# Performance work log

Measured on AMD Instinct MI355X. Metric: run time of the kernel, lower is better.

The kernel has to match this reference:

```python
import jax, jax.numpy as jnp
import numpy as np
from math import comb

N, D, ORDER, P = 32768, 8, 19, 20
O = ORDER + 1


def bernstein(X, order):
    # X: [N, D] in [0,1] -> Bernstein basis [N, D, order+1]
    o = order + 1
    r = jnp.arange(o, dtype=X.dtype)
    binom = jnp.asarray([comb(order, k) for k in range(o)], dtype=X.dtype)
    Xe = X[..., None]
    return (Xe ** r) * ((1.0 - Xe) ** (order - r)) * binom


def setup_inputs() -> dict:
    key = jax.random.key(0)
    k0, k1, k2, k3, k4, k5 = jax.random.split(key, 6)
    X = jax.random.uniform(k0, (N, D), dtype=jnp.float32)
    # perm: each row is a permutation of range(D) (as in the module default)
    perm = jax.vmap(lambda k: jax.random.permutation(k, D))(jax.random.split(k1, P)).astype(jnp.int32)
    meanw0 = -0.2 + 0.1 * jax.random.normal(k2, (P, 1, O), dtype=jnp.float32)
    meanw = -0.2 + 0.1 * jax.random.normal(k3, (D - 1, P, O, O), dtype=jnp.float32)
    varw0 = 0.05 * jax.random.normal(k4, (P, 1, O), dtype=jnp.float32)
    varw = 0.05 * jax.random.normal(k5, (D - 1, P, O, O), dtype=jnp.float32)
    return {"X": X, "perm": perm, "meanw0": meanw0, "meanw": meanw,
            "varw0": varw0, "varw": varw}


def reference(X, perm, meanw0, meanw, varw0, varw):
    outB = bernstein(X, ORDER)                       # [N, D, O]
    outBp = jnp.transpose(outB[:, perm], (1, 0, 2, 3))  # gather axis=1 -> [P, N, D, O]

    # ---- f_mean: chain of small matmuls with exp(meanw_i), gated by basis ----
    f = jnp.exp(meanw0) * outBp[:, :, 0, :]          # [P,1,O]*[P,N,O] -> [P,N,O]
    for i in range(1, D):
        f = jnp.einsum('pno,poq->pnq', f, jnp.exp(meanw[i - 1])) * outBp[:, :, i, :]
    mean = jnp.sum(jnp.sum(f, axis=-1), axis=0)[:, None]   # [N,1]

    # ---- f_var: six moment chains one..six, exp(meanw)^2 * exp(varw)^k ----
    kk = jnp.arange(1, 7, dtype=X.dtype).reshape(6, 1, 1, 1)
    B2_0 = outBp[:, :, 0, :] ** 2                    # [P,N,O]
    acc = jnp.exp(2.0 * meanw0 + kk * varw0) * B2_0[None]  # [6,P,N,O]
    for i in range(1, D):
        Wi = jnp.exp(2.0 * meanw[i - 1] + kk * varw[i - 1])  # [6,P,O,O]
        acc = jnp.einsum('kpno,kpoq->kpnq', acc, Wi) * (outBp[:, :, i, :] ** 2)[None]
    mom = jnp.sum(acc, axis=-1)                      # [6,P,N]
    c = jnp.asarray([1.0, 1 / 2, 1 / 6, 1 / 24, 1 / 120, 1 / 720], dtype=X.dtype)
    var = jnp.einsum('k,kpn->n', c, mom)[:, None]    # [N,1]

    return jnp.concatenate([mean, var], axis=-1)     # [N,2]
```

## Files before the change

### kernel.cpp

```cpp
#include <hip/hip_runtime.h>
#include <math.h>

#define NPTS 32768
#define DD 8
#define OO 20
#define PP 20
#define NCHAIN 7
#define NT 2

typedef _Float16 half8 __attribute__((ext_vector_type(8)));
typedef __fp16 fp16x2 __attribute__((ext_vector_type(2)));
typedef float floatx16 __attribute__((ext_vector_type(16)));
typedef unsigned int u32;

#define AS1 __attribute__((address_space(1)))
#define AS3 __attribute__((address_space(3)))

__device__ __forceinline__ int sigma_row(int m) {
    return (m >= 4 && m < 12) ? (m ^ 12) : m;
}

__device__ __forceinline__ void basis20(float tv, float* g) {
    constexpr float binom[OO] = {
        1.f, 19.f, 171.f, 969.f, 3876.f, 11628.f, 27132.f, 50388.f, 75582.f,
        92378.f, 92378.f, 75582.f, 50388.f, 27132.f, 11628.f, 3876.f, 969.f,
        171.f, 19.f, 1.f};
    float a = tv, b = 1.f - tv, v = 1.f;
#pragma unroll
    for (int q = 0; q < OO; ++q) { g[q] = v; v *= a; }
    v = 1.f;
#pragma unroll
    for (int q = OO - 1; q >= 0; --q) { g[q] = g[q] * v * binom[q]; v *= b; }
}

__device__ __forceinline__ unsigned pk2rtn(float a, float b) {
    union { _Float16 h[2]; unsigned u; } cv;
    cv.h[0] = (_Float16)a; cv.h[1] = (_Float16)b;
    return cv.u;
}

__device__ __forceinline__ unsigned pack_pk(float x, float y) {
    union { fp16x2 h; unsigned u; } cv;
    cv.h = __builtin_amdgcn_cvt_pkrtz(x, y);
    return cv.u;
}

__device__ __forceinline__ fp16x2 u2h(unsigned u) {
    union { unsigned u; fp16x2 h; } c; c.u = u; return c.h;
}
__device__ __forceinline__ unsigned h2u(fp16x2 h) {
    union { unsigned u; fp16x2 h; } c; c.h = h; return c.u;
}

__global__ void zero_kernel(float4* __restrict__ out) {
    int e = blockIdx.x * 256 + threadIdx.x;
    out[e] = make_float4(0.f, 0.f, 0.f, 0.f);
}

__global__ void prep_kernel(const float* __restrict__ X,
                            const float* __restrict__ meanw0,
                            const float* __restrict__ meanw,
                            const float* __restrict__ varw0,
                            const float* __restrict__ varw,
                            float* __restrict__ W0,
                            _Float16* __restrict__ WA,
                            unsigned* __restrict__ G) {
    int e = blockIdx.x * 256 + threadIdx.x;
    const int n0 = NCHAIN * PP * OO;
    const int nW = NCHAIN * (DD - 1) * PP * 32 * 32;
    const int nG = NPTS * DD;
    if (e < n0) {
        int q = e % OO;
        int rem = e / OO;
        int p = rem % PP;
        int c = rem / PP;
        float m = meanw0[p * OO + q];
        W0[e] = (c == 0) ? __expf(m) : __expf(2.f * m + (float)c * varw0[p * OO + q]);
    } else if (e < n0 + nW) {
        int idx = e - n0;
        int j = idx & 7; idx >>= 3;
        int l = idx & 63; idx >>= 6;
        int f = idx & 1; idx >>= 1;
        int p = idx % PP; idx /= PP;
        int i = idx % (DD - 1);
        int c = idx / (DD - 1);
        int m = l & 31;
        int k = (l >> 5) * 8 + f * 16 + j;
        int q = sigma_row(m);
        float v = 0.f;
        if (q < OO && k < OO) {
            int mi = ((i * PP + p) * OO + k) * OO + q;
            float mm = meanw[mi];
            v = (c == 0) ? __expf(mm) : __expf(2.f * mm + (float)c * varw[mi]);
        }
        WA[e - n0] = (_Float16)v;
    } else if (e < n0 + nW + nG) {
        int idx = e - n0 - nW;
        int n = idx & (NPTS - 1);
        int d = idx >> 15;
        float g[OO];
        basis20(X[(size_t)n * DD + d], g);
        uint4 o0, o1, o2;
        o0.x = pk2rtn(g[0], g[1]);
        o0.y = pk2rtn(g[2], g[3]);
        o0.z = pk2rtn(g[4], g[5]);
        o0.w = pk2rtn(g[6], g[7]);
        o1.x = pk2rtn(g[16], g[17]);
        o1.y = pk2rtn(g[18], g[19]);
        o1.z = pk2rtn(g[8], g[9]);
        o1.w = pk2rtn(g[10], g[11]);
        o2.x = pk2rtn(g[12], g[13]);
        o2.y = pk2rtn(g[14], g[15]);
        o2.z = 0u;
        o2.w = 0u;
        uint4* out = (uint4*)(G + (size_t)(d * NPTS + n) * 12);
        out[0] = o0; out[1] = o1; out[2] = o2;
    }
}

__global__ __launch_bounds__(256, 2) void chain_kernel(
    const int* __restrict__ perm,
    const float* __restrict__ W0, const _Float16* __restrict__ WA,
    const unsigned* __restrict__ G, float* __restrict__ out) {
    const int lane = threadIdx.x & 63;
    const int wv = threadIdx.x >> 6;
    const int nl = lane & 31;
    const bool hi = (lane >> 5) != 0;
    const int n0 = (blockIdx.x * 4 + wv) * (32 * NT);
    const int p = blockIdx.y;
    const int goffd = hi ? 6 : 0;

    __shared__ __align__(16) _Float16 Alds[2][NCHAIN * 1024];

    int dp[DD];
#pragma unroll
    for (int i = 0; i < DD; ++i) dp[i] = perm[p * DD + i];

    const unsigned uz = ((unsigned)dp[0]) >> 20;
    const float fz = __uint_as_float(uz);
    floatx16 kZero;
#pragma unroll
    for (int r = 0; r < 16; ++r) kZero[r] = fz;

    {
        const _Float16* wbase = WA + (size_t)p * 1024;
#pragma unroll
        for (int u = wv; u < 2 * NCHAIN; u += 4) {
            int c = u >> 1, h = u & 1;
            const _Float16* src =
                wbase + (size_t)c * (DD - 1) * PP * 1024 + h * 512 + lane * 8;
            __builtin_amdgcn_global_load_lds(
                (const AS1 u32*)src, (AS3 u32*)&Alds[0][u * 512], 16, 0, 0);
        }
    }

    unsigned st[NT][NCHAIN][6];

#pragma unroll
    for (int tile = 0; tile < NT; ++tile) {
        const uint2* rp = (const uint2*)(
            G + ((size_t)dp[0] * NPTS + (n0 + tile * 32 + nl)) * 12 + goffd);
        uint2 r0 = rp[0], r1 = rp[1], r2 = rp[2];
        unsigned gw[6] = {r0.x, r0.y, r1.x, r1.y, r2.x, r2.y};
        float gcf[12], scf[12];
#pragma unroll
        for (int q = 0; q < 6; ++q) {
            fp16x2 gh = u2h(gw[q]);
            gcf[2 * q] = (float)gh.x; gcf[2 * q + 1] = (float)gh.y;
        }
#pragma unroll
        for (int r = 0; r < 12; ++r) scf[r] = gcf[r] * gcf[r];
#pragma unroll
        for (int c = 0; c < NCHAIN; ++c) {
            const float* w0r = W0 + (c * PP + p) * OO;
            float val[12];
#pragma unroll
            for (int r = 0; r < 8; ++r) {
                float ws = hi ? w0r[r + 8] : w0r[r];
                val[r] = ws * (c == 0 ? gcf[r] : scf[r]);
            }
#pragma unroll
            for (int r = 8; r < 12; ++r) {
                float ws = hi ? 0.f : w0r[r + 8];
                val[r] = ws * (c == 0 ? gcf[r] : scf[r]);
            }
#pragma unroll
            for (int e = 0; e < 6; ++e)
                st[tile][c][e] = pack_pk(val[2 * e], val[2 * e + 1]);
        }
    }

    const float coef[NCHAIN] = {0.f, 1.f, 0.5f, 1.f / 6.f, 1.f / 24.f,
                                1.f / 120.f, 1.f / 720.f};
    float sm[NT], sv[NT];
#pragma unroll
    for (int tile = 0; tile < NT; ++tile) { sm[tile] = 0.f; sv[tile] = 0.f; }

    __syncthreads();

#pragma unroll
    for (int i = 1; i < DD; ++i) {
        const int cur = (i - 1) & 1;

        if (i < DD - 1) {
            const _Float16* wbase = WA + (size_t)(i * PP + p) * 1024;
#pragma unroll
            for (int u = wv; u < 2 * NCHAIN; u += 4) {
                int c = u >> 1, h = u & 1;
                const _Float16* src =
                    wbase + (size_t)c * (DD - 1) * PP * 1024 + h * 512 + lane * 8;
                __builtin_amdgcn_global_load_lds(
                    (const AS1 u32*)src, (AS3 u32*)&Alds[cur ^ 1][u * 512], 16, 0, 0);
            }
        }

        unsigned gw[NT][6], sw[NT][6];
#pragma unroll
        for (int tile = 0; tile < NT; ++tile) {
            const uint2* rp = (const uint2*)(
                G + ((size_t)dp[i] * NPTS + (n0 + tile * 32 + nl)) * 12 + goffd);
            uint2 r0 = rp[0], r1 = rp[1], r2 = rp[2];
            gw[tile][0] = r0.x; gw[tile][1] = r0.y;
            gw[tile][2] = r1.x; gw[tile][3] = r1.y;
            gw[tile][4] = r2.x; gw[tile][5] = r2.y;
        }
        if (i < DD - 1) {
#pragma unroll
            for (int tile = 0; tile < NT; ++tile)
#pragma unroll
                for (int e = 0; e < 6; ++e) {
                    fp16x2 gh = u2h(gw[tile][e]);
                    sw[tile][e] = h2u(gh * gh);
                }
        }

        float gcf[NT][12], scf[NT][12];
        if (i == DD - 1) {
#pragma unroll
            for (int tile = 0; tile < NT; ++tile) {
#pragma unroll
                for (int q = 0; q < 6; ++q) {
                    fp16x2 gh = u2h(gw[tile][q]);
                    gcf[tile][2 * q] = (float)gh.x; gcf[tile][2 * q + 1] = (float)gh.y;
                }
#pragma unroll
                for (int r = 0; r < 12; ++r)
                    scf[tile][r] = gcf[tile][r] * gcf[tile][r];
            }
        }

#pragma unroll
        for (int c = 0; c < NCHAIN; ++c) {
            const _Float16* ab = &Alds[cur][c * 1024 + lane * 8];
            half8 A0 = *(const half8*)(ab);
            half8 A1 = *(const half8*)(ab + 512);

#pragma unroll
            for (int tile = 0; tile < NT; ++tile) {
                union { unsigned u[4]; half8 h; } B0, B1;
                B0.u[0] = st[tile][c][0]; B0.u[1] = st[tile][c][1];
                B0.u[2] = st[tile][c][2]; B0.u[3] = st[tile][c][3];
                B1.u[0] = st[tile][c][4]; B1.u[1] = st[tile][c][5];
                B1.u[2] = uz;             B1.u[3] = uz;

                floatx16 acc;
                acc = __builtin_amdgcn_mfma_f32_32x32x16_f16(A0, B0.h, kZero, 0, 0, 0);
                acc = __builtin_amdgcn_mfma_f32_32x32x16_f16(A1, B1.h, acc, 0, 0, 0);

                if (i < DD - 1) {
#pragma unroll
                    for (int e = 0; e < 6; ++e) {
                        fp16x2 pr = __builtin_amdgcn_cvt_pkrtz(acc[2 * e], acc[2 * e + 1]);
                        fp16x2 gv = u2h(c == 0 ? gw[tile][e] : sw[tile][e]);
                        st[tile][c][e] = h2u(pr * gv);
                    }
                } else {
                    float s = 0.f;
#pragma unroll
                    for (int r = 0; r < 12; ++r)
                        s += acc[r] * (c == 0 ? gcf[tile][r] : scf[tile][r]);
                    if (c == 0) sm[tile] = s;
                    else        sv[tile] += coef[c] * s;
                }
            }
        }

        if (i < DD - 1) __syncthreads();
    }

#pragma unroll
    for (int tile = 0; tile < NT; ++tile) {
        float m = sm[tile] + __shfl_xor(sm[tile], 32, 64);
        float v = sv[tile] + __shfl_xor(sv[tile], 32, 64);
        if (lane < 32) {
            int n = n0 + tile * 32 + nl;
            atomicAdd(&out[2 * n], m);
            atomicAdd(&out[2 * n + 1], v);
        }
    }
}

extern "C" void kernel_launch(void* const* d_in, const int* in_sizes, int n_in,
                              void* d_out, int out_size, void* d_ws, size_t ws_size,
                              hipStream_t stream) {
    const float* X      = (const float*)d_in[0];
    const int*   perm   = (const int*)d_in[1];
    const float* meanw0 = (const float*)d_in[2];
    const float* meanw  = (const float*)d_in[3];
    const float* varw0  = (const float*)d_in[4];
    const float* varw   = (const float*)d_in[5];
    float* out = (float*)d_out;

    float*     W0 = (float*)d_ws;
    _Float16*  WA = (_Float16*)((char*)d_ws + 11200);
    unsigned*  G  = (unsigned*)((char*)d_ws + 11200 + 2007040);

    int prep_n = NCHAIN * PP * OO + NCHAIN * (DD - 1) * PP * 32 * 32 + NPTS * DD;
    hipLaunchKernelGGL(prep_kernel, dim3((prep_n + 255) / 256), dim3(256), 0,
                       stream, X, meanw0, meanw, varw0, varw, W0, WA, G);

    hipLaunchKernelGGL(zero_kernel, dim3(2 * NPTS / (4 * 256)), dim3(256), 0,
                       stream, (float4*)out);

    dim3 grid(NPTS / (128 * NT), PP);
    hipLaunchKernelGGL(chain_kernel, grid, dim3(256), 0, stream,
                       perm, W0, WA, G, out);
}
```

Measured before the change: 143.4 us.

## Process five permutations per block with cross-permutation weight prefetch

Each block now loops over a group of five permutations instead of one, and the grid's permutation dimension shrinks accordingly. During the last chain step of one permutation it prefetches the next permutation's first weight tile into LDS and builds its initial state. The goal is to amortize block setup, cut global atomic adds to the output by five, and keep the double-buffered LDS pipeline running across permutations. In exchange the grid has far fewer blocks, so load balancing has less slack, and perm indices are now read from memory inside the loop.

```diff
diff --git a/kernel.cpp b/kernel.cpp
--- a/kernel.cpp
+++ b/kernel.cpp
@@ -7,6 +7,7 @@
 #define PP 20
 #define NCHAIN 7
 #define NT 2
+#define PG 5
 
 typedef _Float16 half8 __attribute__((ext_vector_type(8)));
 typedef __fp16 fp16x2 __attribute__((ext_vector_type(2)));
@@ -118,6 +119,57 @@
     }
 }
 
+#define STAGE_A(pidx, widx, buf)                                               \
+    do {                                                                       \
+        const _Float16* wbase_ = WA + (size_t)((widx) * PP + (pidx)) * 1024;   \
+        _Pragma("unroll")                                                      \
+        for (int u_ = wv; u_ < 2 * NCHAIN; u_ += 4) {                          \
+            int cc_ = u_ >> 1, hh_ = u_ & 1;                                   \
+            const _Float16* src_ = wbase_ +                                    \
+                (size_t)cc_ * (DD - 1) * PP * 1024 + hh_ * 512 + lane * 8;     \
+            __builtin_amdgcn_global_load_lds((const AS1 u32*)src_,             \
+                (AS3 u32*)&Alds[buf][u_ * 512], 16, 0, 0);                     \
+        }                                                                      \
+    } while (0)
+
+#define INIT_ST(pidx)                                                          \
+    do {                                                                       \
+        int d0_ = perm[(pidx) * DD];                                           \
+        _Pragma("unroll")                                                      \
+        for (int tile = 0; tile < NT; ++tile) {                                \
+            const uint2* rp_ = (const uint2*)(G +                              \
+                ((size_t)d0_ * NPTS + (n0 + tile * 32 + nl)) * 12 + goffd);    \
+            uint2 r0_ = rp_[0], r1_ = rp_[1], r2_ = rp_[2];                    \
+            unsigned gwv_[6] = {r0_.x, r0_.y, r1_.x, r1_.y, r2_.x, r2_.y};     \
+            float gcf_[12], scf_[12];                                          \
+            _Pragma("unroll")                                                  \
+            for (int q_ = 0; q_ < 6; ++q_) {                                   \
+                fp16x2 gh_ = u2h(gwv_[q_]);                                    \
+                gcf_[2 * q_] = (float)gh_.x; gcf_[2 * q_ + 1] = (float)gh_.y;  \
+            }                                                                  \
+            _Pragma("unroll")                                                  \
+            for (int r_ = 0; r_ < 12; ++r_) scf_[r_] = gcf_[r_] * gcf_[r_];    \
+            _Pragma("unroll")                                                  \
+            for (int c = 0; c < NCHAIN; ++c) {                                 \
+                const float* w0r_ = W0 + (c * PP + (pidx)) * OO;               \
+                float val_[12];                                                \
+                _Pragma("unroll")                                              \
+                for (int r_ = 0; r_ < 8; ++r_) {                               \
+                    float ws_ = hi ? w0r_[r_ + 8] : w0r_[r_];                  \
+                    val_[r_] = ws_ * (c == 0 ? gcf_[r_] : scf_[r_]);           \
+                }                                                              \
+                _Pragma("unroll")                                              \
+                for (int r_ = 8; r_ < 12; ++r_) {                              \
+                    float ws_ = hi ? 0.f : w0r_[r_ + 8];                       \
+                    val_[r_] = ws_ * (c == 0 ? gcf_[r_] : scf_[r_]);           \
+                }                                                              \
+                _Pragma("unroll")                                              \
+                for (int e_ = 0; e_ < 6; ++e_)                                 \
+                    st[tile][c][e_] = pack_pk(val_[2 * e_], val_[2 * e_ + 1]); \
+            }                                                                  \
+        }                                                                      \
+    } while (0)
+
 __global__ __launch_bounds__(256, 2) void chain_kernel(
     const int* __restrict__ perm,
     const float* __restrict__ W0, const _Float16* __restrict__ WA,
@@ -127,171 +179,123 @@
     const int nl = lane & 31;
     const bool hi = (lane >> 5) != 0;
     const int n0 = (blockIdx.x * 4 + wv) * (32 * NT);
-    const int p = blockIdx.y;
+    const int pBeg = blockIdx.y * PG;
     const int goffd = hi ? 6 : 0;
 
     __shared__ __align__(16) _Float16 Alds[2][NCHAIN * 1024];
 
-    int dp[DD];
-#pragma unroll
-    for (int i = 0; i < DD; ++i) dp[i] = perm[p * DD + i];
-
-    const unsigned uz = ((unsigned)dp[0]) >> 20;
+    const unsigned uz = ((unsigned)perm[pBeg * DD]) >> 20;
     const float fz = __uint_as_float(uz);
     floatx16 kZero;
 #pragma unroll
     for (int r = 0; r < 16; ++r) kZero[r] = fz;
 
-    {
-        const _Float16* wbase = WA + (size_t)p * 1024;
-#pragma unroll
-        for (int u = wv; u < 2 * NCHAIN; u += 4) {
-            int c = u >> 1, h = u & 1;
-            const _Float16* src =
-                wbase + (size_t)c * (DD - 1) * PP * 1024 + h * 512 + lane * 8;
-            __builtin_amdgcn_global_load_lds(
-                (const AS1 u32*)src, (AS3 u32*)&Alds[0][u * 512], 16, 0, 0);
+    unsigned st[NT][NCHAIN][6];
+    const float coef[NCHAIN] = {0.f, 1.f, 0.5f, 1.f / 6.f, 1.f / 24.f,
+                                1.f / 120.f, 1.f / 720.f};
+    float smT[NT], svT[NT];
+#pragma unroll
+    for (int tile = 0; tile < NT; ++tile) { smT[tile] = 0.f; svT[tile] = 0.f; }
+
+    STAGE_A(pBeg, 0, 0);
+    INIT_ST(pBeg);
+    __syncthreads();
+
+    int cur = 0;
+    for (int pp = pBeg; pp < pBeg + PG; ++pp) {
+#pragma unroll
+        for (int i = 1; i < DD; ++i) {
+            if (i < DD - 1) {
+                STAGE_A(pp, i, cur ^ 1);
+            } else if (pp + 1 < pBeg + PG) {
+                STAGE_A(pp + 1, 0, cur ^ 1);
+            }
+
+            const int di = perm[pp * DD + i];
+            unsigned gw[NT][6], sw[NT][6];
+#pragma unroll
+            for (int tile = 0; tile < NT; ++tile) {
+                const uint2* rp = (const uint2*)(
+                    G + ((size_t)di * NPTS + (n0 + tile * 32 + nl)) * 12 + goffd);
+                uint2 r0 = rp[0], r1 = rp[1], r2 = rp[2];
+                gw[tile][0] = r0.x; gw[tile][1] = r0.y;
+                gw[tile][2] = r1.x; gw[tile][3] = r1.y;
+                gw[tile][4] = r2.x; gw[tile][5] = r2.y;
+            }
+            if (i < DD - 1) {
+#pragma unroll
+                for (int tile = 0; tile < NT; ++tile)
+#pragma unroll
+                    for (int e = 0; e < 6; ++e) {
+                        fp16x2 gh = u2h(gw[tile][e]);
+                        sw[tile][e] = h2u(gh * gh);
+                    }
+            }
+
+            float gcf[NT][12], scf[NT][12];
+            if (i == DD - 1) {
+#pragma unroll
+                for (int tile = 0; tile < NT; ++tile) {
+#pragma unroll
+                    for (int q = 0; q < 6; ++q) {
+                        fp16x2 gh = u2h(gw[tile][q]);
+                        gcf[tile][2 * q] = (float)gh.x;
+                        gcf[tile][2 * q + 1] = (float)gh.y;
+                    }
+#pragma unroll
+                    for (int r = 0; r < 12; ++r)
+                        scf[tile][r] = gcf[tile][r] * gcf[tile][r];
+                }
+            }
+
+#pragma unroll
+            for (int c = 0; c < NCHAIN; ++c) {
+                const _Float16* ab = &Alds[cur][c * 1024 + lane * 8];
+                half8 A0 = *(const half8*)(ab);
+                half8 A1 = *(const half8*)(ab + 512);
+
+#pragma unroll
+                for (int tile = 0; tile < NT; ++tile) {
+                    union { unsigned u[4]; half8 h; } B0, B1;
+                    B0.u[0] = st[tile][c][0]; B0.u[1] = st[tile][c][1];
+                    B0.u[2] = st[tile][c][2]; B0.u[3] = st[tile][c][3];
+                    B1.u[0] = st[tile][c][4]; B1.u[1] = st[tile][c][5];
+                    B1.u[2] = uz;             B1.u[3] = uz;
+
+                    floatx16 acc;
+                    acc = __builtin_amdgcn_mfma_f32_32x32x16_f16(A0, B0.h, kZero, 0, 0, 0);
+                    acc = __builtin_amdgcn_mfma_f32_32x32x16_f16(A1, B1.h, acc, 0, 0, 0);
+
+                    if (i < DD - 1) {
+#pragma unroll
+                        for (int e = 0; e < 6; ++e) {
+                            fp16x2 pr = __builtin_amdgcn_cvt_pkrtz(acc[2 * e], acc[2 * e + 1]);
+                            fp16x2 gv = u2h(c == 0 ? gw[tile][e] : sw[tile][e]);
+                            st[tile][c][e] = h2u(pr * gv);
+                        }
+                    } else {
+                        float s = 0.f;
+#pragma unroll
+                        for (int r = 0; r < 12; ++r)
+                            s += acc[r] * (c == 0 ? gcf[tile][r] : scf[tile][r]);
+                        if (c == 0) smT[tile] += s;
+                        else        svT[tile] += coef[c] * s;
+                    }
+                }
+            }
+
+            if (i == DD - 1 && pp + 1 < pBeg + PG) INIT_ST(pp + 1);
+
+            if (!(i == DD - 1 && pp == pBeg + PG - 1))
+                __syncthreads();
+            cur ^= 1;
         }
     }
 
-    unsigned st[NT][NCHAIN][6];
-
 #pragma unroll
     for (int tile = 0; tile < NT; ++tile) {
-        const uint2* rp = (const uint2*)(
-            G + ((size_t)dp[0] * NPTS + (n0 + tile * 32 + nl)) * 12 + goffd);
-        uint2 r0 = rp[0], r1 = rp[1], r2 = rp[2];
-        unsigned gw[6] = {r0.x, r0.y, r1.x, r1.y, r2.x, r2.y};
-        float gcf[12], scf[12];
-#pragma unroll
-        for (int q = 0; q < 6; ++q) {
-            fp16x2 gh = u2h(gw[q]);
-            gcf[2 * q] = (float)gh.x; gcf[2 * q + 1] = (float)gh.y;
-        }
-#pragma unroll
-        for (int r = 0; r < 12; ++r) scf[r] = gcf[r] * gcf[r];
-#pragma unroll
-        for (int c = 0; c < NCHAIN; ++c) {
-            const float* w0r = W0 + (c * PP + p) * OO;
-            float val[12];
-#pragma unroll
-            for (int r = 0; r < 8; ++r) {
-                float ws = hi ? w0r[r + 8] : w0r[r];
-                val[r] = ws * (c == 0 ? gcf[r] : scf[r]);
-            }
-#pragma unroll
-            for (int r = 8; r < 12; ++r) {
-                float ws = hi ? 0.f : w0r[r + 8];
-                val[r] = ws * (c == 0 ? gcf[r] : scf[r]);
-            }
-#pragma unroll
-            for (int e = 0; e < 6; ++e)
-                st[tile][c][e] = pack_pk(val[2 * e], val[2 * e + 1]);
-        }
-    }
-
-    const float coef[NCHAIN] = {0.f, 1.f, 0.5f, 1.f / 6.f, 1.f / 24.f,
-                                1.f / 120.f, 1.f / 720.f};
-    float sm[NT], sv[NT];
-#pragma unroll
-    for (int tile = 0; tile < NT; ++tile) { sm[tile] = 0.f; sv[tile] = 0.f; }
-
-    __syncthreads();
-
-#pragma unroll
-    for (int i = 1; i < DD; ++i) {
-        const int cur = (i - 1) & 1;
-
-        if (i < DD - 1) {
-            const _Float16* wbase = WA + (size_t)(i * PP + p) * 1024;
-#pragma unroll
-            for (int u = wv; u < 2 * NCHAIN; u += 4) {
-                int c = u >> 1, h = u & 1;
-                const _Float16* src =
-                    wbase + (size_t)c * (DD - 1) * PP * 1024 + h * 512 + lane * 8;
-                __builtin_amdgcn_global_load_lds(
-                    (const AS1 u32*)src, (AS3 u32*)&Alds[cur ^ 1][u * 512], 16, 0, 0);
-            }
-        }
-
-        unsigned gw[NT][6], sw[NT][6];
-#pragma unroll
-        for (int tile = 0; tile < NT; ++tile) {
-            const uint2* rp = (const uint2*)(
-                G + ((size_t)dp[i] * NPTS + (n0 + tile * 32 + nl)) * 12 + goffd);
-            uint2 r0 = rp[0], r1 = rp[1], r2 = rp[2];
-            gw[tile][0] = r0.x; gw[tile][1] = r0.y;
-            gw[tile][2] = r1.x; gw[tile][3] = r1.y;
-            gw[tile][4] = r2.x; gw[tile][5] = r2.y;
-        }
-        if (i < DD - 1) {
-#pragma unroll
-            for (int tile = 0; tile < NT; ++tile)
-#pragma unroll
-                for (int e = 0; e < 6; ++e) {
-                    fp16x2 gh = u2h(gw[tile][e]);
-                    sw[tile][e] = h2u(gh * gh);
-                }
-        }
-
-        float gcf[NT][12], scf[NT][12];
-        if (i == DD - 1) {
-#pragma unroll
-            for (int tile = 0; tile < NT; ++tile) {
-#pragma unroll
-                for (int q = 0; q < 6; ++q) {
-                    fp16x2 gh = u2h(gw[tile][q]);
-                    gcf[tile][2 * q] = (float)gh.x; gcf[tile][2 * q + 1] = (float)gh.y;
-                }
-#pragma unroll
-                for (int r = 0; r < 12; ++r)
-                    scf[tile][r] = gcf[tile][r] * gcf[tile][r];
-            }
-        }
-
-#pragma unroll
-        for (int c = 0; c < NCHAIN; ++c) {
-            const _Float16* ab = &Alds[cur][c * 1024 + lane * 8];
-            half8 A0 = *(const half8*)(ab);
-            half8 A1 = *(const half8*)(ab + 512);
-
-#pragma unroll
-            for (int tile = 0; tile < NT; ++tile) {
-                union { unsigned u[4]; half8 h; } B0, B1;
-                B0.u[0] = st[tile][c][0]; B0.u[1] = st[tile][c][1];
-                B0.u[2] = st[tile][c][2]; B0.u[3] = st[tile][c][3];
-                B1.u[0] = st[tile][c][4]; B1.u[1] = st[tile][c][5];
-                B1.u[2] = uz;             B1.u[3] = uz;
-
-                floatx16 acc;
-                acc = __builtin_amdgcn_mfma_f32_32x32x16_f16(A0, B0.h, kZero, 0, 0, 0);
-                acc = __builtin_amdgcn_mfma_f32_32x32x16_f16(A1, B1.h, acc, 0, 0, 0);
-
-                if (i < DD - 1) {
-#pragma unroll
-                    for (int e = 0; e < 6; ++e) {
-                        fp16x2 pr = __builtin_amdgcn_cvt_pkrtz(acc[2 * e], acc[2 * e + 1]);
-                        fp16x2 gv = u2h(c == 0 ? gw[tile][e] : sw[tile][e]);
-                        st[tile][c][e] = h2u(pr * gv);
-                    }
-                } else {
-                    float s = 0.f;
-#pragma unroll
-                    for (int r = 0; r < 12; ++r)
-                        s += acc[r] * (c == 0 ? gcf[tile][r] : scf[tile][r]);
-                    if (c == 0) sm[tile] = s;
-                    else        sv[tile] += coef[c] * s;
-                }
-            }
-        }
-
-        if (i < DD - 1) __syncthreads();
-    }
-
-#pragma unroll
-    for (int tile = 0; tile < NT; ++tile) {
-        float m = sm[tile] + __shfl_xor(sm[tile], 32, 64);
-        float v = sv[tile] + __shfl_xor(sv[tile], 32, 64);
+        float m = smT[tile] + __shfl_xor(smT[tile], 32, 64);
+        float v = svT[tile] + __shfl_xor(svT[tile], 32, 64);
         if (lane < 32) {
             int n = n0 + tile * 32 + nl;
             atomicAdd(&out[2 * n], m);
@@ -322,7 +326,7 @@
     hipLaunchKernelGGL(zero_kernel, dim3(2 * NPTS / (4 * 256)), dim3(256), 0,
                        stream, (float4*)out);
 
-    dim3 grid(NPTS / (128 * NT), PP);
+    dim3 grid(NPTS / (128 * NT), PP / PG);
     hipLaunchKernelGGL(chain_kernel, grid, dim3(256), 0, stream,
                        perm, W0, WA, G, out);
 }
```

Result: slower. 384.0 us (+167.8%).
